# Optimization experiments

Hardware: AMD Instinct MI355X
Metric: run time of the kernel (lower is better)

The kernel has to match this reference:

```python
import jax, jax.numpy as jnp
import numpy as np

ALPHA = 0.2          # LeakyReLU slope
THRESH = 0.6         # adjacency connection threshold
NEG_INF = -9e15      # masked-softmax fill used by the original


def setup_inputs() -> dict:
    key = jax.random.key(0)
    ks = jax.random.split(key, 5)
    B, N, F = 32, 512, 128
    h = jax.random.normal(ks[0], (B, N, F), dtype=jnp.float32)
    # torch nn.Linear weights: y = x @ W.T
    W = jax.random.normal(ks[1], (F, F), dtype=jnp.float32) * 0.1
    a = jax.random.normal(ks[2], (2 * F, 1), dtype=jnp.float32) * 0.1
    A0 = jax.random.normal(ks[3], (4 * N, N), dtype=jnp.float32) * 0.05
    A2 = jax.random.normal(ks[4], (N, 4 * N), dtype=jnp.float32) * 0.05
    return {"h": h, "W": W, "a": a, "A0": A0, "A2": A2}


def reference(h, W, a, A0, A2):
    F = W.shape[0]
    # Wh = W(h)                                  [B, N, F]
    Wh = jnp.einsum("bnf,gf->bng", h, W)
    # attention logits e = leakyrelu(Wh a1 + (Wh a2)^T)   [B, N, N]
    Wh1 = Wh @ a[:F]                              # [B, N, 1]
    Wh2 = Wh @ a[F:]                              # [B, N, 1]
    e = jax.nn.leaky_relu(Wh1 + jnp.swapaxes(Wh2, 1, 2), ALPHA)
    # learned adjacency MLP over last (node) dim: Linear -> Sigmoid -> Linear
    adj = e + jnp.einsum("bnk,mk->bnm", jax.nn.sigmoid(jnp.einsum("bnm,km->bnk", e, A0)), A2)
    # threshold + mask + softmax
    adj = jnp.where(adj > THRESH, adj, 0.0)
    att = jnp.where(adj > 0, e, NEG_INF)
    att = jax.nn.softmax(att, axis=2)
    # dropout is identity in eval mode
    h_prime = jnp.einsum("bnm,bmf->bnf", att, Wh)
    return jax.nn.elu(h_prime)                    # concat=True branch
```

## Files before the change

kernel.cpp:

```cpp
#include <hip/hip_runtime.h>

#define BB 32
#define NN 512
#define FF 128
#define K4 2048
#define ALPHA 0.2f
#define THRESH 0.6f
#define NEGINF -9e15f

typedef unsigned short u16;
typedef unsigned int u32;
typedef _Float16 f16;
typedef __attribute__((ext_vector_type(8))) _Float16 half8;
typedef __attribute__((ext_vector_type(4))) float f32x4;

union U16F { u16 u; f16 h; };
__device__ __forceinline__ u16 hbits(f16 h) { U16F x; x.h = h; return x.u; }
__device__ __forceinline__ float htof(u16 u) { U16F x; x.u = u; return (float)x.h; }
__device__ __forceinline__ void split2(float v, u16& hi, u16& lo) {
    f16 h = (f16)v;
    f16 l = (f16)(v - (float)h);
    hi = hbits(h);
    lo = hbits(l);
}
__device__ __forceinline__ float lrelu(float x) { return fmaxf(x, ALPHA * x); }

__device__ __forceinline__ void gload16(const void* g, void* l) {
    __builtin_amdgcn_global_load_lds(
        (__attribute__((address_space(1))) const unsigned int*)(unsigned long long)g,
        (__attribute__((address_space(3))) unsigned int*)(unsigned int)(unsigned long long)l,
        16, 0, 0);
}

__global__ void k_u(const float* __restrict__ W, const float* __restrict__ a,
                    float* __restrict__ u12) {
    int f = threadIdx.x;
    float s1 = 0.f, s2 = 0.f;
    for (int g = 0; g < FF; ++g) {
        float w = W[g * FF + f];
        s1 += w * a[g];
        s2 += w * a[FF + g];
    }
    u12[f] = s1;
    u12[FF + f] = s2;
}

__global__ void k_wh12(const float* __restrict__ h, const float* __restrict__ u12,
                       float* __restrict__ Wh12) {
    int row = blockIdx.x;
    int f = threadIdx.x;
    float hv = h[(size_t)row * FF + f];
    float p1 = hv * u12[f], p2 = hv * u12[FF + f];
#pragma unroll
    for (int o = 1; o < 64; o <<= 1) {
        p1 += __shfl_xor(p1, o, 64);
        p2 += __shfl_xor(p2, o, 64);
    }
    __shared__ float s1[2], s2[2];
    int w = f >> 6;
    if ((f & 63) == 0) { s1[w] = p1; s2[w] = p2; }
    __syncthreads();
    if (f == 0) {
        Wh12[row] = s1[0] + s1[1];
        Wh12[BB * NN + row] = s2[0] + s2[1];
    }
}

__global__ __launch_bounds__(256) void k_whT(const float* __restrict__ W,
                                             const float* __restrict__ h,
                                             u16* __restrict__ Thi, u16* __restrict__ Tlo) {
    const int bm = blockIdx.y * 64, bn = blockIdx.x * 64;
    __shared__ float As[32][68];
    __shared__ float Bs[32][68];
    int tid = threadIdx.x;
    int tx = tid & 15, ty = tid >> 4;
    float acc[4][4] = {{0.f}};
    int r = tid >> 3, q = tid & 7;
    const float* Ap = W + (size_t)(bm + r) * FF + q * 4;
    const float* Bp = h + (size_t)(bn + r) * FF + q * 4;
    for (int k0 = 0; k0 < FF; k0 += 32) {
        float4 a0 = *(const float4*)(Ap + k0);
        float4 a1 = *(const float4*)(Ap + k0 + 32 * FF);
        float4 b0 = *(const float4*)(Bp + k0);
        float4 b1 = *(const float4*)(Bp + k0 + 32 * FF);
        __syncthreads();
        As[q * 4 + 0][r] = a0.x; As[q * 4 + 1][r] = a0.y;
        As[q * 4 + 2][r] = a0.z; As[q * 4 + 3][r] = a0.w;
        As[q * 4 + 0][r + 32] = a1.x; As[q * 4 + 1][r + 32] = a1.y;
        As[q * 4 + 2][r + 32] = a1.z; As[q * 4 + 3][r + 32] = a1.w;
        Bs[q * 4 + 0][r] = b0.x; Bs[q * 4 + 1][r] = b0.y;
        Bs[q * 4 + 2][r] = b0.z; Bs[q * 4 + 3][r] = b0.w;
        Bs[q * 4 + 0][r + 32] = b1.x; Bs[q * 4 + 1][r + 32] = b1.y;
        Bs[q * 4 + 2][r + 32] = b1.z; Bs[q * 4 + 3][r + 32] = b1.w;
        __syncthreads();
#pragma unroll
        for (int kk = 0; kk < 32; ++kk) {
            float av[4], bv[4];
            *(float4*)av = *(const float4*)&As[kk][ty * 4];
            *(float4*)bv = *(const float4*)&Bs[kk][tx * 4];
#pragma unroll
            for (int i = 0; i < 4; ++i)
#pragma unroll
                for (int j = 0; j < 4; ++j) acc[i][j] = fmaf(av[i], bv[j], acc[i][j]);
        }
    }
#pragma unroll
    for (int i = 0; i < 4; ++i) {
        int f = bm + ty * 4 + i;
#pragma unroll
        for (int j = 0; j < 4; ++j) {
            int mg = bn + tx * 4 + j;
            u16 hi, lo;
            split2(acc[i][j], hi, lo);
            size_t idx = ((size_t)(mg >> 9) * FF + f) * NN + (mg & 511);
            Thi[idx] = hi;
            Tlo[idx] = lo;
        }
    }
}

__global__ void k_split(const float* __restrict__ X, u16* __restrict__ Hi,
                        u16* __restrict__ Lo, int n4) {
    int i = blockIdx.x * 256 + threadIdx.x;
    if (i >= n4) return;
    float4 v = *(const float4*)(X + (size_t)i * 4);
    ushort4 hh, ll;
    split2(v.x, hh.x, ll.x);
    split2(v.y, hh.y, ll.y);
    split2(v.z, hh.z, ll.z);
    split2(v.w, hh.w, ll.w);
    *(ushort4*)(Hi + (size_t)i * 4) = hh;
    *(ushort4*)(Lo + (size_t)i * 4) = ll;
}

__global__ __launch_bounds__(512, 2) void k_g1(const float* __restrict__ Wh12, int c0,
                                               const u16* __restrict__ Bhi,
                                               const u16* __restrict__ Blo,
                                               u16* __restrict__ Shi, u16* __restrict__ Slo,
                                               int mblocks) {
    __shared__ __align__(16) u16 lds[2][4][8192];
    __shared__ float wh1s[256];
    __shared__ float wh2s[512];
    const int tid = threadIdx.x;
    const int l = tid & 63, w = tid >> 6;
    const int p = w >> 2, wq = w & 3;
    const int nwg = gridDim.x, q = nwg >> 3;
    const int wg = (blockIdx.x & 7) * q + (blockIdx.x >> 3);
    const int nb = wg / mblocks, mb = wg % mblocks;
    const int bm = mb * 256, bn = nb * 256;
    const int bglob = c0 + (bm >> 9);

    if (tid < 256) wh1s[tid] = Wh12[(size_t)c0 * NN + bm + tid];
    wh2s[tid] = Wh12[BB * NN + (size_t)bglob * NN + tid];
    __syncthreads();

    f32x4 acc[8][4];
#pragma unroll
    for (int m = 0; m < 8; ++m)
#pragma unroll
        for (int n = 0; n < 4; ++n) acc[m][n] = (f32x4){0.f, 0.f, 0.f, 0.f};

    auto STAGE_MINE = [&](int buf, int k0) {
#pragma unroll
        for (int i = 0; i < 2; ++i) {
            const int g = p * 8 + wq * 2 + i;
            const size_t ro = (size_t)(bn + g * 16 + (l & 15)) * NN + k0 + ((l >> 4) * 8);
            gload16(Bhi + ro, &lds[buf][2][g * 512]);
            gload16(Blo + ro, &lds[buf][3][g * 512]);
        }
    };
    auto GEN_MINE = [&](int buf, int k0) {
        const int kc = k0 + (l >> 4) * 8;
        float w2v[8];
        *(float4*)&w2v[0] = *(const float4*)&wh2s[kc];
        *(float4*)&w2v[4] = *(const float4*)&wh2s[kc + 4];
#pragma unroll
        for (int i = 0; i < 2; ++i) {
            const int g = p * 8 + wq * 2 + i;
            const float w1 = wh1s[g * 16 + (l & 15)];
            u32 hh[4], llv[4];
#pragma unroll
            for (int jj = 0; jj < 4; ++jj) {
                float e0 = lrelu(w1 + w2v[2 * jj]);
                float e1 = lrelu(w1 + w2v[2 * jj + 1]);
                u16 h0, l0, h1, l1;
                split2(e0, h0, l0);
                split2(e1, h1, l1);
                hh[jj] = (u32)h0 | ((u32)h1 << 16);
                llv[jj] = (u32)l0 | ((u32)l1 << 16);
            }
            *(uint4*)&lds[buf][0][(g * 64 + l) * 8] = make_uint4(hh[0], hh[1], hh[2], hh[3]);
            *(uint4*)&lds[buf][1][(g * 64 + l) * 8] = make_uint4(llv[0], llv[1], llv[2], llv[3]);
        }
    };
    auto DO_MFMA = [&](int cur) {
        half8 bh[4], bl[4];
#pragma unroll
        for (int n = 0; n < 4; ++n) {
            const int gB = wq * 4 + n;
            bh[n] = *(const half8*)&lds[cur][2][(gB * 64 + l) * 8];
            bl[n] = *(const half8*)&lds[cur][3][(gB * 64 + l) * 8];
        }
        __builtin_amdgcn_s_setprio(1);
#pragma unroll
        for (int m = 0; m < 8; ++m) {
            const int gA = p * 8 + m;
            half8 ah = *(const half8*)&lds[cur][0][(gA * 64 + l) * 8];
            half8 al = *(const half8*)&lds[cur][1][(gA * 64 + l) * 8];
#pragma unroll
            for (int n = 0; n < 4; ++n)
                acc[m][n] = __builtin_amdgcn_mfma_f32_16x16x32_f16(ah, bh[n], acc[m][n], 0, 0, 0);
#pragma unroll
            for (int n = 0; n < 4; ++n)
                acc[m][n] = __builtin_amdgcn_mfma_f32_16x16x32_f16(al, bh[n], acc[m][n], 0, 0, 0);
#pragma unroll
            for (int n = 0; n < 4; ++n)
                acc[m][n] = __builtin_amdgcn_mfma_f32_16x16x32_f16(ah, bl[n], acc[m][n], 0, 0, 0);
        }
        __builtin_amdgcn_s_setprio(0);
    };

    STAGE_MINE(0, 0);
    GEN_MINE(0, 0);
    asm volatile("s_waitcnt vmcnt(0) lgkmcnt(0)" ::: "memory");
    __syncthreads();

    for (int t = 0; t < 16; ++t) {
        const int cur = t & 1, k1 = (t + 1) * 32;
        const bool more = (t < 15);
        if (more) STAGE_MINE(cur ^ 1, k1);
        if (p == 0) DO_MFMA(cur);
        else if (more) GEN_MINE(cur ^ 1, k1);
        asm volatile("s_waitcnt lgkmcnt(0)" ::: "memory");
        __builtin_amdgcn_s_barrier();
        if (p == 1) DO_MFMA(cur);
        else if (more) GEN_MINE(cur ^ 1, k1);
        asm volatile("s_waitcnt vmcnt(0) lgkmcnt(0)" ::: "memory");
        __builtin_amdgcn_s_barrier();
    }

    const int lr = (l >> 4) * 4, lc = l & 15;
#pragma unroll
    for (int m = 0; m < 8; ++m) {
#pragma unroll
        for (int n = 0; n < 4; ++n) {
#pragma unroll
            for (int j = 0; j < 4; ++j) {
                const int row = bm + p * 128 + m * 16 + lr + j;
                const int col = bn + wq * 64 + n * 16 + lc;
                const float s = 1.f / (1.f + __expf(-acc[m][n][j]));
                u16 hi, lo;
                split2(s, hi, lo);
                const size_t idx = (size_t)row * K4 + col;
                Shi[idx] = hi;
                Slo[idx] = lo;
            }
        }
    }
}

__global__ __launch_bounds__(512, 2) void k_g2(const u16* __restrict__ Ahi,
                                               const u16* __restrict__ Alo,
                                               const u16* __restrict__ Bhi,
                                               const u16* __restrict__ Blo,
                                               const float* __restrict__ Wh12, int c0,
                                               u32* __restrict__ ADJ, int mblocks) {
    __shared__ __align__(16) u16 ldsA[2][2][4096];
    __shared__ __align__(16) u16 ldsB[2][2][8192];
    const int tid = threadIdx.x;
    const int l = tid & 63, w = tid >> 6;
    const int nwg = gridDim.x, q = nwg >> 3;
    const int wg = (blockIdx.x & 7) * q + (blockIdx.x >> 3);
    const int nb = wg / mblocks, mb = wg % mblocks;
    const int bm = mb * 128, bn = nb * 256;

    auto STAGE = [&](int buf, int k0) {
        const size_t ra = (size_t)(bm + w * 16 + (l & 15)) * K4 + k0 + ((l >> 4) * 8);
        gload16(Ahi + ra, &ldsA[buf][0][w * 512]);
        gload16(Alo + ra, &ldsA[buf][1][w * 512]);
#pragma unroll
        for (int i = 0; i < 2; ++i) {
            const int g = w * 2 + i;
            const size_t rb = (size_t)(bn + g * 16 + (l & 15)) * K4 + k0 + ((l >> 4) * 8);
            gload16(Bhi + rb, &ldsB[buf][0][g * 512]);
            gload16(Blo + rb, &ldsB[buf][1][g * 512]);
        }
    };

    f32x4 acc[4][4];
#pragma unroll
    for (int m = 0; m < 4; ++m)
#pragma unroll
        for (int n = 0; n < 4; ++n) acc[m][n] = (f32x4){0.f, 0.f, 0.f, 0.f};

    STAGE(0, 0);
    for (int t = 0; t < 64; ++t) {
        const int cur = t & 1;
        if (t < 63) {
            STAGE(cur ^ 1, (t + 1) * 32);
            asm volatile("s_waitcnt vmcnt(6)" ::: "memory");
        } else {
            asm volatile("s_waitcnt vmcnt(0)" ::: "memory");
        }
        __builtin_amdgcn_s_barrier();
        __builtin_amdgcn_sched_barrier(0);
        half8 bh[4], bl[4];
#pragma unroll
        for (int n = 0; n < 4; ++n) {
            const int gB = (w & 3) * 4 + n;
            bh[n] = *(const half8*)&ldsB[cur][0][(gB * 64 + l) * 8];
            bl[n] = *(const half8*)&ldsB[cur][1][(gB * 64 + l) * 8];
        }
        __builtin_amdgcn_s_setprio(1);
#pragma unroll
        for (int m = 0; m < 4; ++m) {
            const int gA = (w >> 2) * 4 + m;
            half8 ah = *(const half8*)&ldsA[cur][0][(gA * 64 + l) * 8];
            half8 al = *(const half8*)&ldsA[cur][1][(gA * 64 + l) * 8];
#pragma unroll
            for (int n = 0; n < 4; ++n)
                acc[m][n] = __builtin_amdgcn_mfma_f32_16x16x32_f16(ah, bh[n], acc[m][n], 0, 0, 0);
#pragma unroll
            for (int n = 0; n < 4; ++n)
                acc[m][n] = __builtin_amdgcn_mfma_f32_16x16x32_f16(al, bh[n], acc[m][n], 0, 0, 0);
#pragma unroll
            for (int n = 0; n < 4; ++n)
                acc[m][n] = __builtin_amdgcn_mfma_f32_16x16x32_f16(ah, bl[n], acc[m][n], 0, 0, 0);
        }
        __builtin_amdgcn_s_setprio(0);
        __builtin_amdgcn_sched_barrier(0);
        __builtin_amdgcn_s_barrier();
    }

    const int bglob = c0 + (bm >> 9);
    const float* wh2p = Wh12 + BB * NN + (size_t)bglob * NN;
    const int lr = (l >> 4) * 4, lc = l & 15;
#pragma unroll
    for (int m = 0; m < 4; ++m) {
#pragma unroll
        for (int n = 0; n < 4; ++n) {
#pragma unroll
            for (int j = 0; j < 4; ++j) {
                const int row = bm + (w >> 2) * 64 + m * 16 + lr + j;
                const int col = bn + (w & 3) * 64 + n * 16 + lc;
                const float e = lrelu(Wh12[(size_t)c0 * NN + row] + wh2p[col]);
                u32 pk = 0xFFFFFFFFu;
                if (e + acc[m][n][j] > THRESH) {
                    u16 hi, lo;
                    split2(e, hi, lo);
                    pk = (u32)hi | ((u32)lo << 16);
                }
                ADJ[(size_t)row * NN + col] = pk;
            }
        }
    }
}

__global__ __launch_bounds__(256) void k_softmax2(const u32* __restrict__ ADJ,
                                                  u16* __restrict__ Hi, u16* __restrict__ Lo) {
    const size_t row = blockIdx.x;
    const u32* p = ADJ + row * NN;
    const int t = threadIdx.x;
    u32 w0 = p[t], w1 = p[t + 256];
    float v0 = (w0 == 0xFFFFFFFFu) ? NEGINF : htof((u16)(w0 & 0xFFFF)) + htof((u16)(w0 >> 16));
    float v1 = (w1 == 0xFFFFFFFFu) ? NEGINF : htof((u16)(w1 & 0xFFFF)) + htof((u16)(w1 >> 16));
    float m = fmaxf(v0, v1);
#pragma unroll
    for (int o = 1; o < 64; o <<= 1) m = fmaxf(m, __shfl_xor(m, o, 64));
    __shared__ float red[4], red2[4];
    int w = t >> 6;
    if ((t & 63) == 0) red[w] = m;
    __syncthreads();
    m = fmaxf(fmaxf(red[0], red[1]), fmaxf(red[2], red[3]));
    float e0 = __expf(v0 - m), e1 = __expf(v1 - m);
    float s = e0 + e1;
#pragma unroll
    for (int o = 1; o < 64; o <<= 1) s += __shfl_xor(s, o, 64);
    if ((t & 63) == 0) red2[w] = s;
    __syncthreads();
    s = red2[0] + red2[1] + red2[2] + red2[3];
    float inv = 1.f / s;
    float a0 = e0 * inv, a1 = e1 * inv;
    u16 h0, l0, h1, l1;
    split2(a0, h0, l0);
    split2(a1, h1, l1);
    Hi[row * NN + t] = h0;
    Hi[row * NN + t + 256] = h1;
    Lo[row * NN + t] = l0;
    Lo[row * NN + t + 256] = l1;
}

__global__ __launch_bounds__(256) void k_pv(const u16* __restrict__ Ahi,
                                            const u16* __restrict__ Alo,
                                            const u16* __restrict__ Bhi,
                                            const u16* __restrict__ Blo,
                                            float* __restrict__ OUT) {
    __shared__ __align__(16) u16 lds[2][4][4096];
    const int tid = threadIdx.x;
    const int l = tid & 63, w = tid >> 6;
    const int wr = w >> 1, wc = w & 1;
    const int bz = blockIdx.z;
    const int bm = blockIdx.y * 128, bn = 0;

    const u16* A0p = Ahi + (size_t)bz * NN * NN;
    const u16* A1p = Alo + (size_t)bz * NN * NN;
    const u16* B0p = Bhi + (size_t)bz * FF * NN;
    const u16* B1p = Blo + (size_t)bz * FF * NN;

    const int g0 = w, g1 = w + 4;
    const size_t offA0 = (size_t)(bm + g0 * 16 + (l & 15)) * NN + (l >> 4) * 8;
    const size_t offA1 = (size_t)(bm + g1 * 16 + (l & 15)) * NN + (l >> 4) * 8;
    const size_t offB0 = (size_t)(bn + g0 * 16 + (l & 15)) * NN + (l >> 4) * 8;
    const size_t offB1 = (size_t)(bn + g1 * 16 + (l & 15)) * NN + (l >> 4) * 8;

    auto STAGE = [&](int buf, int kk) {
        gload16(A0p + offA0 + kk, &lds[buf][0][g0 * 512]);
        gload16(A0p + offA1 + kk, &lds[buf][0][g1 * 512]);
        gload16(A1p + offA0 + kk, &lds[buf][1][g0 * 512]);
        gload16(A1p + offA1 + kk, &lds[buf][1][g1 * 512]);
        gload16(B0p + offB0 + kk, &lds[buf][2][g0 * 512]);
        gload16(B0p + offB1 + kk, &lds[buf][2][g1 * 512]);
        gload16(B1p + offB0 + kk, &lds[buf][3][g0 * 512]);
        gload16(B1p + offB1 + kk, &lds[buf][3][g1 * 512]);
    };

    f32x4 acc[4][4];
#pragma unroll
    for (int m = 0; m < 4; ++m)
#pragma unroll
        for (int n = 0; n < 4; ++n) acc[m][n] = (f32x4){0.f, 0.f, 0.f, 0.f};

    STAGE(0, 0);
    for (int t = 0; t < 16; ++t) {
        const int cur = t & 1;
        if (t + 1 < 16) {
            STAGE(cur ^ 1, (t + 1) * 32);
            asm volatile("s_waitcnt vmcnt(8)" ::: "memory");
        } else {
            asm volatile("s_waitcnt vmcnt(0)" ::: "memory");
        }
        __builtin_amdgcn_s_barrier();
        __builtin_amdgcn_sched_barrier(0);
        half8 ah[4], al[4], bh[4], bl[4];
#pragma unroll
        for (int m = 0; m < 4; ++m) {
            ah[m] = *(const half8*)&lds[cur][0][((wr * 4 + m) * 64 + l) * 8];
            al[m] = *(const half8*)&lds[cur][1][((wr * 4 + m) * 64 + l) * 8];
        }
#pragma unroll
        for (int n = 0; n < 4; ++n) {
            bh[n] = *(const half8*)&lds[cur][2][((wc * 4 + n) * 64 + l) * 8];
            bl[n] = *(const half8*)&lds[cur][3][((wc * 4 + n) * 64 + l) * 8];
        }
#pragma unroll
        for (int m = 0; m < 4; ++m) {
#pragma unroll
            for (int n = 0; n < 4; ++n)
                acc[m][n] = __builtin_amdgcn_mfma_f32_16x16x32_f16(ah[m], bh[n], acc[m][n], 0, 0, 0);
        }
#pragma unroll
        for (int m = 0; m < 4; ++m) {
#pragma unroll
            for (int n = 0; n < 4; ++n) {
                acc[m][n] = __builtin_amdgcn_mfma_f32_16x16x32_f16(al[m], bh[n], acc[m][n], 0, 0, 0);
                acc[m][n] = __builtin_amdgcn_mfma_f32_16x16x32_f16(ah[m], bl[n], acc[m][n], 0, 0, 0);
            }
        }
        __builtin_amdgcn_s_barrier();
    }

    const int lr = (l >> 4) * 4, lc = l & 15;
#pragma unroll
    for (int m = 0; m < 4; ++m) {
#pragma unroll
        for (int n = 0; n < 4; ++n) {
#pragma unroll
            for (int j = 0; j < 4; ++j) {
                const int row = bm + wr * 64 + m * 16 + lr + j;
                const int col = bn + wc * 64 + n * 16 + lc;
                const float v = acc[m][n][j];
                OUT[(size_t)bz * NN * FF + (size_t)row * FF + col] =
                    v > 0.f ? v : __expf(v) - 1.f;
            }
        }
    }
}

extern "C" void kernel_launch(void* const* d_in, const int* in_sizes, int n_in,
                              void* d_out, int out_size, void* d_ws, size_t ws_size,
                              hipStream_t stream) {
    const float* h = (const float*)d_in[0];
    const float* W = (const float*)d_in[1];
    const float* a = (const float*)d_in[2];
    const float* A0 = (const float*)d_in[3];
    const float* A2 = (const float*)d_in[4];
    float* out = (float*)d_out;

    char* ws = (char*)d_ws;
    size_t ofs = 0;
    auto alloc = [&](size_t bytes) -> void* {
        void* p = ws + ofs;
        ofs = (ofs + bytes + 255) & ~(size_t)255;
        return p;
    };
    float* u12 = (float*)alloc(2 * FF * sizeof(float));
    float* Wh12 = (float*)alloc(2 * (size_t)BB * NN * sizeof(float));
    u16* WhThi = (u16*)alloc((size_t)BB * FF * NN * 2);
    u16* WhTlo = (u16*)alloc((size_t)BB * FF * NN * 2);
    u16* A0hi = (u16*)alloc((size_t)K4 * NN * 2);
    u16* A0lo = (u16*)alloc((size_t)K4 * NN * 2);
    u16* A2hi = (u16*)alloc((size_t)NN * K4 * 2);
    u16* A2lo = (u16*)alloc((size_t)NN * K4 * 2);

    const size_t per_b =
        (size_t)NN * K4 * 2 * 2 + (size_t)NN * NN * 4 + (size_t)NN * NN * 2 * 2;
    int cb = BB;
    while (cb > 1 && ofs + (size_t)cb * per_b + 8192 > ws_size) cb >>= 1;
    u16* Shi = (u16*)alloc((size_t)cb * NN * K4 * 2);
    u16* Slo = (u16*)alloc((size_t)cb * NN * K4 * 2);
    u32* ADJ = (u32*)alloc((size_t)cb * NN * NN * 4);
    u16* AttHi = (u16*)alloc((size_t)cb * NN * NN * 2);
    u16* AttLo = (u16*)alloc((size_t)cb * NN * NN * 2);

    k_u<<<1, 128, 0, stream>>>(W, a, u12);
    k_wh12<<<BB * NN, 128, 0, stream>>>(h, u12, Wh12);
    k_whT<<<dim3((BB * NN) / 64, FF / 64), 256, 0, stream>>>(W, h, WhThi, WhTlo);
    k_split<<<(K4 * NN / 4 + 255) / 256, 256, 0, stream>>>(A0, A0hi, A0lo, K4 * NN / 4);
    k_split<<<(NN * K4 / 4 + 255) / 256, 256, 0, stream>>>(A2, A2hi, A2lo, NN * K4 / 4);

    for (int c0 = 0; c0 < BB; c0 += cb) {
        const int c = (BB - c0) < cb ? (BB - c0) : cb;
        const int mb1 = c * 2;
        const int mb2 = c * 4;
        k_g1<<<mb1 * (K4 / 256), 512, 0, stream>>>(Wh12, c0, A0hi, A0lo, Shi, Slo, mb1);
        k_g2<<<mb2 * (NN / 256), 512, 0, stream>>>(Shi, Slo, A2hi, A2lo, Wh12, c0, ADJ, mb2);
        k_softmax2<<<c * NN, 256, 0, stream>>>(ADJ, AttHi, AttLo);
        k_pv<<<dim3(1, NN / 128, c), 256, 0, stream>>>(
            AttHi, AttLo, WhThi + (size_t)c0 * FF * NN, WhTlo + (size_t)c0 * FF * NN,
            out + (size_t)c0 * NN * FF);
    }
}
```

Baseline: 282.3 us.

## Shrink k_g1 tile to 128 rows with simple sync loop, alias Att buffers onto S

k_g1 moves from a 256x256 tile with double-buffered, warp-specialized generate/MFMA ping-pong to a 128x256 tile where every wave both generates its slice of the A operand and runs MFMAs, with plain __syncthreads between single-buffered stages. This halves accumulator registers and LDS use and doubles the grid, giving more waves per CU, but loses the overlap of generation, loads and compute. The softmax output buffers now reuse the Shi/Slo workspace instead of separate allocations, which shrinks per-batch workspace so larger batch chunks fit.

```diff
diff --git a/kernel.cpp b/kernel.cpp
--- a/kernel.cpp
+++ b/kernel.cpp
@@ -133,80 +133,83 @@
     *(ushort4*)(Lo + (size_t)i * 4) = ll;
 }
 
-__global__ __launch_bounds__(512, 2) void k_g1(const float* __restrict__ Wh12, int c0,
-                                               const u16* __restrict__ Bhi,
-                                               const u16* __restrict__ Blo,
-                                               u16* __restrict__ Shi, u16* __restrict__ Slo,
-                                               int mblocks) {
-    __shared__ __align__(16) u16 lds[2][4][8192];
-    __shared__ float wh1s[256];
+__global__ __launch_bounds__(512) void k_g1(const float* __restrict__ Wh12, int c0,
+                                            const u16* __restrict__ Bhi,
+                                            const u16* __restrict__ Blo,
+                                            u16* __restrict__ Shi, u16* __restrict__ Slo,
+                                            int mblocks) {
+    __shared__ __align__(16) u16 ldsA[8192];
+    __shared__ __align__(16) u16 ldsB[16384];
+    __shared__ float wh1s[128];
     __shared__ float wh2s[512];
     const int tid = threadIdx.x;
     const int l = tid & 63, w = tid >> 6;
-    const int p = w >> 2, wq = w & 3;
+    const int wm = w >> 2, wn = w & 3;
     const int nwg = gridDim.x, q = nwg >> 3;
     const int wg = (blockIdx.x & 7) * q + (blockIdx.x >> 3);
     const int nb = wg / mblocks, mb = wg % mblocks;
-    const int bm = mb * 256, bn = nb * 256;
+    const int bm = mb * 128, bn = nb * 256;
     const int bglob = c0 + (bm >> 9);
 
-    if (tid < 256) wh1s[tid] = Wh12[(size_t)c0 * NN + bm + tid];
-    wh2s[tid] = Wh12[BB * NN + (size_t)bglob * NN + tid];
+    if (tid < 128) wh1s[tid] = Wh12[(size_t)c0 * NN + bm + tid];
+    if (tid < 512) wh2s[tid] = Wh12[BB * NN + (size_t)bglob * NN + tid];
+
+    f32x4 acc[4][4];
+#pragma unroll
+    for (int m = 0; m < 4; ++m)
+#pragma unroll
+        for (int n = 0; n < 4; ++n) acc[m][n] = (f32x4){0.f, 0.f, 0.f, 0.f};
+
+    const int gb0 = w * 2, gb1 = w * 2 + 1;
+    const size_t rb0 = (size_t)(bn + gb0 * 16 + (l & 15)) * NN + ((l >> 4) * 8);
+    const size_t rb1 = (size_t)(bn + gb1 * 16 + (l & 15)) * NN + ((l >> 4) * 8);
+    const int arow = (tid >> 6) * 16 + (l & 15);
+    const int akc = (l >> 4) * 8;
+    const float w1 = wh1s[0];
+
     __syncthreads();
-
-    f32x4 acc[8][4];
-#pragma unroll
-    for (int m = 0; m < 8; ++m)
-#pragma unroll
-        for (int n = 0; n < 4; ++n) acc[m][n] = (f32x4){0.f, 0.f, 0.f, 0.f};
-
-    auto STAGE_MINE = [&](int buf, int k0) {
-#pragma unroll
-        for (int i = 0; i < 2; ++i) {
-            const int g = p * 8 + wq * 2 + i;
-            const size_t ro = (size_t)(bn + g * 16 + (l & 15)) * NN + k0 + ((l >> 4) * 8);
-            gload16(Bhi + ro, &lds[buf][2][g * 512]);
-            gload16(Blo + ro, &lds[buf][3][g * 512]);
-        }
-    };
-    auto GEN_MINE = [&](int buf, int k0) {
-        const int kc = k0 + (l >> 4) * 8;
-        float w2v[8];
-        *(float4*)&w2v[0] = *(const float4*)&wh2s[kc];
-        *(float4*)&w2v[4] = *(const float4*)&wh2s[kc + 4];
-#pragma unroll
-        for (int i = 0; i < 2; ++i) {
-            const int g = p * 8 + wq * 2 + i;
-            const float w1 = wh1s[g * 16 + (l & 15)];
+    (void)w1;
+
+    const float myw1 = wh1s[arow];
+
+    for (int t = 0; t < 16; ++t) {
+        const int k0 = t * 32;
+        gload16(Bhi + rb0 + k0, &ldsB[gb0 * 512]);
+        gload16(Bhi + rb1 + k0, &ldsB[gb1 * 512]);
+        gload16(Blo + rb0 + k0, &ldsB[8192 + gb0 * 512]);
+        gload16(Blo + rb1 + k0, &ldsB[8192 + gb1 * 512]);
+        {
+            const int kc = k0 + akc;
+            float w2v[8];
+            *(float4*)&w2v[0] = *(const float4*)&wh2s[kc];
+            *(float4*)&w2v[4] = *(const float4*)&wh2s[kc + 4];
             u32 hh[4], llv[4];
 #pragma unroll
             for (int jj = 0; jj < 4; ++jj) {
-                float e0 = lrelu(w1 + w2v[2 * jj]);
-                float e1 = lrelu(w1 + w2v[2 * jj + 1]);
+                float e0 = lrelu(myw1 + w2v[2 * jj]);
+                float e1 = lrelu(myw1 + w2v[2 * jj + 1]);
                 u16 h0, l0, h1, l1;
                 split2(e0, h0, l0);
                 split2(e1, h1, l1);
                 hh[jj] = (u32)h0 | ((u32)h1 << 16);
                 llv[jj] = (u32)l0 | ((u32)l1 << 16);
             }
-            *(uint4*)&lds[buf][0][(g * 64 + l) * 8] = make_uint4(hh[0], hh[1], hh[2], hh[3]);
-            *(uint4*)&lds[buf][1][(g * 64 + l) * 8] = make_uint4(llv[0], llv[1], llv[2], llv[3]);
-        }
-    };
-    auto DO_MFMA = [&](int cur) {
+            *(uint4*)&ldsA[tid * 8] = make_uint4(hh[0], hh[1], hh[2], hh[3]);
+            *(uint4*)&ldsA[4096 + tid * 8] = make_uint4(llv[0], llv[1], llv[2], llv[3]);
+        }
+        __syncthreads();
         half8 bh[4], bl[4];
 #pragma unroll
         for (int n = 0; n < 4; ++n) {
-            const int gB = wq * 4 + n;
-            bh[n] = *(const half8*)&lds[cur][2][(gB * 64 + l) * 8];
-            bl[n] = *(const half8*)&lds[cur][3][(gB * 64 + l) * 8];
-        }
-        __builtin_amdgcn_s_setprio(1);
-#pragma unroll
-        for (int m = 0; m < 8; ++m) {
-            const int gA = p * 8 + m;
-            half8 ah = *(const half8*)&lds[cur][0][(gA * 64 + l) * 8];
-            half8 al = *(const half8*)&lds[cur][1][(gA * 64 + l) * 8];
+            const int gB = wn * 4 + n;
+            bh[n] = *(const half8*)&ldsB[(gB * 64 + l) * 8];
+            bl[n] = *(const half8*)&ldsB[8192 + (gB * 64 + l) * 8];
+        }
+#pragma unroll
+        for (int m = 0; m < 4; ++m) {
+            const int gA = wm * 4 + m;
+            half8 ah = *(const half8*)&ldsA[(gA * 64 + l) * 8];
+            half8 al = *(const half8*)&ldsA[4096 + (gA * 64 + l) * 8];
 #pragma unroll
             for (int n = 0; n < 4; ++n)
                 acc[m][n] = __builtin_amdgcn_mfma_f32_16x16x32_f16(ah, bh[n], acc[m][n], 0, 0, 0);
@@ -217,37 +220,18 @@
             for (int n = 0; n < 4; ++n)
                 acc[m][n] = __builtin_amdgcn_mfma_f32_16x16x32_f16(ah, bl[n], acc[m][n], 0, 0, 0);
         }
-        __builtin_amdgcn_s_setprio(0);
-    };
-
-    STAGE_MINE(0, 0);
-    GEN_MINE(0, 0);
-    asm volatile("s_waitcnt vmcnt(0) lgkmcnt(0)" ::: "memory");
-    __syncthreads();
-
-    for (int t = 0; t < 16; ++t) {
-        const int cur = t & 1, k1 = (t + 1) * 32;
-        const bool more = (t < 15);
-        if (more) STAGE_MINE(cur ^ 1, k1);
-        if (p == 0) DO_MFMA(cur);
-        else if (more) GEN_MINE(cur ^ 1, k1);
-        asm volatile("s_waitcnt lgkmcnt(0)" ::: "memory");
-        __builtin_amdgcn_s_barrier();
-        if (p == 1) DO_MFMA(cur);
-        else if (more) GEN_MINE(cur ^ 1, k1);
-        asm volatile("s_waitcnt vmcnt(0) lgkmcnt(0)" ::: "memory");
-        __builtin_amdgcn_s_barrier();
+        __syncthreads();
     }
 
     const int lr = (l >> 4) * 4, lc = l & 15;
 #pragma unroll
-    for (int m = 0; m < 8; ++m) {
+    for (int m = 0; m < 4; ++m) {
 #pragma unroll
         for (int n = 0; n < 4; ++n) {
 #pragma unroll
             for (int j = 0; j < 4; ++j) {
-                const int row = bm + p * 128 + m * 16 + lr + j;
-                const int col = bn + wq * 64 + n * 16 + lc;
+                const int row = bm + wm * 64 + m * 16 + lr + j;
+                const int col = bn + wn * 64 + n * 16 + lc;
                 const float s = 1.f / (1.f + __expf(-acc[m][n][j]));
                 u16 hi, lo;
                 split2(s, hi, lo);
@@ -512,15 +496,14 @@
     u16* A2hi = (u16*)alloc((size_t)NN * K4 * 2);
     u16* A2lo = (u16*)alloc((size_t)NN * K4 * 2);
 
-    const size_t per_b =
-        (size_t)NN * K4 * 2 * 2 + (size_t)NN * NN * 4 + (size_t)NN * NN * 2 * 2;
+    const size_t per_b = (size_t)NN * K4 * 2 * 2 + (size_t)NN * NN * 4;
     int cb = BB;
     while (cb > 1 && ofs + (size_t)cb * per_b + 8192 > ws_size) cb >>= 1;
     u16* Shi = (u16*)alloc((size_t)cb * NN * K4 * 2);
     u16* Slo = (u16*)alloc((size_t)cb * NN * K4 * 2);
     u32* ADJ = (u32*)alloc((size_t)cb * NN * NN * 4);
-    u16* AttHi = (u16*)alloc((size_t)cb * NN * NN * 2);
-    u16* AttLo = (u16*)alloc((size_t)cb * NN * NN * 2);
+    u16* AttHi = Shi;
+    u16* AttLo = Slo;
 
     k_u<<<1, 128, 0, stream>>>(W, a, u12);
     k_wh12<<<BB * NN, 128, 0, stream>>>(h, u12, Wh12);
@@ -530,7 +513,7 @@
 
     for (int c0 = 0; c0 < BB; c0 += cb) {
         const int c = (BB - c0) < cb ? (BB - c0) : cb;
-        const int mb1 = c * 2;
+        const int mb1 = c * 4;
         const int mb2 = c * 4;
         k_g1<<<mb1 * (K4 / 256), 512, 0, stream>>>(Wh12, c0, A0hi, A0lo, Shi, Slo, mb1);
         k_g2<<<mb2 * (NN / 256), 512, 0, stream>>>(Shi, Slo, A2hi, A2lo, Wh12, c0, ADJ, mb2);
```

Result: slower. 292.4 us (+3.6%).
